# Kernel tuning notes

Measured on AMD Instinct MI355X. Metric: run time of the kernel, lower is better.

Reference implementation:

```python
import jax, jax.numpy as jnp
import numpy as np

CPG = 2          # channels_per_group
WH, WW = 227, 227  # window_size
EPS = 1e-05


def setup_inputs() -> dict:
    key = jax.random.key(0)
    x = jax.random.normal(key, (8, 32, 512, 512), dtype=jnp.float32)
    weight = jnp.ones((1, 32, 1, 1), dtype=jnp.float32)
    bias = jnp.zeros((1, 32, 1, 1), dtype=jnp.float32)
    return {"x": x, "weight": weight, "bias": bias}


def _box_sum(ii, wh, ww):
    # ii: integral image (N,C,H,W); returns window sums of size (wh,ww)
    # over rows h+1..h+wh, cols w+1..w+ww -> (N,C,H-wh,W-ww)
    return (ii[:, :, wh:, ww:] - ii[:, :, :-wh, ww:]
            - ii[:, :, wh:, :-ww] + ii[:, :, :-wh, :-ww])


def reference(x, weight, bias):
    N, C, H, W = x.shape
    G = C // CPG
    # window_size (227,227) < (H,W)=(512,512): integral-image branch
    ii = jnp.cumsum(jnp.cumsum(x, axis=2), axis=3)
    ii_sq = jnp.cumsum(jnp.cumsum(x * x, axis=2), axis=3)
    h, w = H - WH, W - WW
    # per-channel box sums, then sum over channels_per_group -> (N,G,h,w)
    sums = _box_sum(ii, WH, WW).reshape(N, G, CPG, h, w).sum(axis=2)
    squares = _box_sum(ii_sq, WH, WW).reshape(N, G, CPG, h, w).sum(axis=2)
    n = WH * WW * CPG
    means = sums / n
    var = (squares - sums * sums / n) / n
    # replicate-pad stats back to (H,W): (left,right,top,bottom) like F.pad
    pt, pb = (H - h) // 2, H - h - (H - h) // 2
    pl, pr = (W - w) // 2, W - w - (W - w) // 2
    pad = ((0, 0), (0, 0), (pt, pb), (pl, pr))
    p_means = jnp.pad(means, pad, mode='edge')
    p_vars = jnp.pad(var, pad, mode='edge') + EPS
    # torch computes sums/squares under no_grad -> stats are constants
    p_means = jax.lax.stop_gradient(p_means)
    p_vars = jax.lax.stop_gradient(p_vars)
    xg = x.reshape(N, G, CPG, H, W)
    out = (xg - p_means[:, :, None]) / jnp.sqrt(p_vars)[:, :, None]
    out = out.reshape(N, C, H, W)
    return out * weight + bias
```

## Files before the change

kernel.cpp:

```cpp
#include <hip/hip_runtime.h>

namespace {
constexpr int Hn = 512, Wn = 512;
constexpr int WHn = 227, WWn = 227;
constexpr int OHn = 285, OWn = 285;
constexpr int PTn = 113, PLn = 113;
constexpr float EPSn = 1e-5f;
constexpr int NSEG = 17, NSLOT = 9;
__device__ __constant__ int kSegA[NSEG] =
    {1,37,73,109,145,181,217,228,253,264,285,300,336,372,408,444,480};
__device__ __constant__ int kSegB[NSEG] =
    {36,72,108,144,180,216,227,252,263,284,299,335,371,407,443,479,511};
__device__ __constant__ int kWinLo[NSLOT] = {0,1,2,3,4,5,6,8,10};
__device__ __constant__ int kWinHi[NSLOT] = {6,8,10,11,12,13,14,15,16};
__device__ __constant__ int kBr0[8] = {0,29,57,85,398,427,456,484};
__device__ __constant__ int kBrN[8] = {29,28,28,28,29,29,28,28};
}

__global__ __launch_bounds__(512, 4) void lcn_snap(const float* __restrict__ x,
                                                   float2* __restrict__ snap) {
  const int B = blockIdx.x;
  const int g = B >> 2;
  const int st = B & 3;
  const int w = threadIdx.x;
  const int q2 = w & 31;
  const int p = w >> 5;

  const float4* __restrict__ b0 =
      reinterpret_cast<const float4*>(x + (size_t)(g * 2) * Hn * Wn) + st * 32 + q2;
  const float4* __restrict__ b1 = b0 + (size_t)Hn * (Wn / 4);

  __shared__ float4 tbuf[16][64];
  __shared__ float2 segLds[NSEG][128];

  for (int s = 0; s < NSEG; ++s) {
    float4 aS = {0.f,0.f,0.f,0.f}, aQ = {0.f,0.f,0.f,0.f};
    for (int r = kSegA[s] + p; r <= kSegB[s]; r += 16) {
      float4 a = b0[(size_t)r * (Wn / 4)];
      float4 b = b1[(size_t)r * (Wn / 4)];
      aS.x += a.x + b.x; aQ.x += a.x * a.x + b.x * b.x;
      aS.y += a.y + b.y; aQ.y += a.y * a.y + b.y * b.y;
      aS.z += a.z + b.z; aQ.z += a.z * a.z + b.z * b.z;
      aS.w += a.w + b.w; aQ.w += a.w * a.w + b.w * b.w;
    }
    __syncthreads();
    tbuf[p][2 * q2]     = make_float4(aS.x, aQ.x, aS.y, aQ.y);
    tbuf[p][2 * q2 + 1] = make_float4(aS.z, aQ.z, aS.w, aQ.w);
    __syncthreads();
    if (w < 128) {
      const float2* cf = reinterpret_cast<const float2*>(&tbuf[0][0]);
      float2 acc = {0.f, 0.f};
      #pragma unroll
      for (int pp = 0; pp < 16; ++pp) {
        float2 t = cf[pp * 128 + w];
        acc.x += t.x; acc.y += t.y;
      }
      segLds[s][w] = acc;
    }
  }
  __syncthreads();
  if (w < 128) {
    for (int k = 0; k < NSLOT; ++k) {
      float2 acc = {0.f, 0.f};
      for (int i = kWinLo[k]; i <= kWinHi[k]; ++i) {
        acc.x += segLds[i][w].x; acc.y += segLds[i][w].y;
      }
      snap[((size_t)g * NSLOT + k) * 512 + st * 128 + w] = acc;
    }
  }
}

__global__ __launch_bounds__(512, 4) void lcn_fused(const float* __restrict__ x,
                                                    const float* __restrict__ weight,
                                                    const float* __restrict__ bias,
                                                    const float2* __restrict__ snap,
                                                    float* __restrict__ out) {
  const int B = blockIdx.x;
  const int X = B & 7;
  const int s = B >> 3;
  const int chunk = s & 7;
  const int g = X * 16 + (s >> 3);
  const int w = threadIdx.x;
  const int lane = w & 63;
  const int wid = w >> 6;

  const float* __restrict__ x0 = x + (size_t)(g * 2) * Hn * Wn;
  const float* __restrict__ x1 = x0 + (size_t)Hn * Wn;
  float* __restrict__ o0 = out + (size_t)(g * 2) * Hn * Wn;
  float* __restrict__ o1 = o0 + (size_t)Hn * Wn;
  const int cch = (g & 15) * 2;
  const float wt0 = weight[cch], wt1 = weight[cch + 1];
  const float bs0 = bias[cch], bs1 = bias[cch + 1];

  const int h0 = chunk * 36;
  const int h1 = min(OHn, h0 + 36);

  __shared__ __align__(16) float2 Ps[2][4][Wn + 1];
  __shared__ float2 wsum[8][4];

  const float2 sv = snap[((size_t)g * NSLOT + chunk) * 512 + w];
  float accS = sv.x, accQ = sv.y;
  const int bslot = (chunk < 4) ? 0 : 8;
  const float2 bv = snap[((size_t)g * NSLOT + bslot) * 512 + w];

  const float inv_n = 1.0f / (float)(WHn * WWn * 2);
  const int wp = min(max(w - PLn, 0), OWn - 1);

  float pa0[4], pa1[4], ps0[4], ps1[4];
  auto prefetch = [&](int hb) {
    #pragma unroll
    for (int j = 0; j < 4; ++j) {
      int ra = min(hb + WHn + 1 + j, Hn - 1);
      int rs = hb + 1 + j;
      pa0[j] = x0[(size_t)ra * Wn + w];
      pa1[j] = x1[(size_t)ra * Wn + w];
      ps0[j] = x0[(size_t)rs * Wn + w];
      ps1[j] = x1[(size_t)rs * Wn + w];
    }
  };
  prefetch(h0);

  int buf = 0;
  for (int h = h0; h < h1; h += 4) {
    float2 v[4];
    v[0] = make_float2(accS, accQ);
    float s2 = accS, q2 = accQ;
    #pragma unroll
    for (int j = 0; j < 3; ++j) {
      s2 += (pa0[j] + pa1[j]) - (ps0[j] + ps1[j]);
      q2 += (pa0[j] * pa0[j] + pa1[j] * pa1[j])
          - (ps0[j] * ps0[j] + ps1[j] * ps1[j]);
      v[j + 1] = make_float2(s2, q2);
    }
    s2 += (pa0[3] + pa1[3]) - (ps0[3] + ps1[3]);
    q2 += (pa0[3] * pa0[3] + pa1[3] * pa1[3])
        - (ps0[3] * ps0[3] + ps1[3] * ps1[3]);
    accS = s2; accQ = q2;

    if (h + 4 < h1) prefetch(h + 4);
    float xa[4], xb[4];
    #pragma unroll
    for (int rr = 0; rr < 4; ++rr) {
      const size_t hh = (size_t)(h + PTn + rr) * Wn + w;
      xa[rr] = x0[hh];
      xb[rr] = x1[hh];
    }

    #pragma unroll
    for (int d = 1; d < 64; d <<= 1) {
      #pragma unroll
      for (int rr = 0; rr < 4; ++rr) {
        float sx = __shfl_up(v[rr].x, d, 64);
        float sy = __shfl_up(v[rr].y, d, 64);
        if (lane >= d) { v[rr].x += sx; v[rr].y += sy; }
      }
    }
    if (lane == 63) {
      #pragma unroll
      for (int rr = 0; rr < 4; ++rr) wsum[wid][rr] = v[rr];
    }
    __syncthreads();
    float2 off[4] = {{0.f,0.f},{0.f,0.f},{0.f,0.f},{0.f,0.f}};
    #pragma unroll
    for (int i = 0; i < 7; ++i) {
      if (i < wid) {
        #pragma unroll
        for (int rr = 0; rr < 4; ++rr) {
          off[rr].x += wsum[i][rr].x; off[rr].y += wsum[i][rr].y;
        }
      }
    }
    #pragma unroll
    for (int rr = 0; rr < 4; ++rr)
      Ps[buf][rr][w + 1] = make_float2(v[rr].x + off[rr].x, v[rr].y + off[rr].y);
    __syncthreads();

    #pragma unroll
    for (int rr = 0; rr < 4; ++rr) {
      if (h + rr < h1) {
        float2 hi = Ps[buf][rr][wp + WWn + 1];
        float2 lo = Ps[buf][rr][wp + 1];
        float S = hi.x - lo.x;
        float Q = hi.y - lo.y;
        float mean = S * inv_n;
        float var = (Q - S * S * inv_n) * inv_n;
        float istd = rsqrtf(var + EPSn);
        const size_t oo = (size_t)(h + PTn + rr) * Wn + w;
        o0[oo] = (xa[rr] - mean) * istd * wt0 + bs0;
        o1[oo] = (xb[rr] - mean) * istd * wt1 + bs1;
      }
    }
    buf ^= 1;
  }

  __syncthreads();
  {
    float2 v = bv;
    #pragma unroll
    for (int d = 1; d < 64; d <<= 1) {
      float sx = __shfl_up(v.x, d, 64);
      float sy = __shfl_up(v.y, d, 64);
      if (lane >= d) { v.x += sx; v.y += sy; }
    }
    if (lane == 63) wsum[wid][0] = v;
    __syncthreads();
    float2 off = {0.f, 0.f};
    #pragma unroll
    for (int i = 0; i < 7; ++i) {
      if (i < wid) { off.x += wsum[i][0].x; off.y += wsum[i][0].y; }
    }
    Ps[0][0][w + 1] = make_float2(v.x + off.x, v.y + off.y);
    __syncthreads();
    float2 hi = Ps[0][0][wp + WWn + 1];
    float2 lo = Ps[0][0][wp + 1];
    float S = hi.x - lo.x;
    float Q = hi.y - lo.y;
    float mean = S * inv_n;
    float var = (Q - S * S * inv_n) * inv_n;
    float istd = rsqrtf(var + EPSn);
    Ps[0][1][w] = make_float2(mean, istd);
    __syncthreads();
  }
  {
    const float2* bst = &Ps[0][1][0];
    const int row0 = kBr0[chunk];
    const int total = kBrN[chunk] * 256;
    const float4* __restrict__ xf0 = reinterpret_cast<const float4*>(x0);
    const float4* __restrict__ xf1 = reinterpret_cast<const float4*>(x1);
    float4* __restrict__ of0 = reinterpret_cast<float4*>(o0);
    float4* __restrict__ of1 = reinterpret_cast<float4*>(o1);
    for (int i = w; i < total; i += 512) {
      const int qq = i & 127;
      const int ch = (i >> 7) & 1;
      const int row = row0 + (i >> 8);
      const size_t idx = (size_t)row * (Wn / 4) + qq;
      const float4 xv = ch ? xf1[idx] : xf0[idx];
      const float wt = ch ? wt1 : wt0;
      const float bsv = ch ? bs1 : bs0;
      const float2 m0 = bst[4 * qq + 0];
      const float2 m1 = bst[4 * qq + 1];
      const float2 m2 = bst[4 * qq + 2];
      const float2 m3 = bst[4 * qq + 3];
      float4 ov;
      ov.x = (xv.x - m0.x) * m0.y * wt + bsv;
      ov.y = (xv.y - m1.x) * m1.y * wt + bsv;
      ov.z = (xv.z - m2.x) * m2.y * wt + bsv;
      ov.w = (xv.w - m3.x) * m3.y * wt + bsv;
      if (ch) of1[idx] = ov; else of0[idx] = ov;
    }
  }
}

extern "C" void kernel_launch(void* const* d_in, const int* in_sizes, int n_in,
                              void* d_out, int out_size, void* d_ws, size_t ws_size,
                              hipStream_t stream) {
  const float* x = (const float*)d_in[0];
  const float* weight = (const float*)d_in[1];
  const float* bias = (const float*)d_in[2];
  float* out = (float*)d_out;
  float2* snap = (float2*)d_ws;

  hipLaunchKernelGGL(lcn_snap, dim3(512), dim3(512), 0, stream, x, snap);
  hipLaunchKernelGGL(lcn_fused, dim3(1024), dim3(512), 0, stream,
                     x, weight, bias, snap, out);
}
```

Before: 180.8 us.

## Write padded border rows from prefetched sliding-window registers instead of re-reading

The replicate-padded top and bottom border rows are now computed inside the main sliding-window loop, reusing the rows already prefetched for the running-sum update instead of running a separate epilogue pass that re-reads x for those rows. The border mean/istd is computed once up front, and row 0 is handled separately by chunk 0. The snap kernel's column reduction loop is also unrolled by two to keep more loads in flight. This removes redundant global reads, but the border stores are now scattered per row inside the loop and are only done by the chunks that happen to cover those rows.

```diff
diff --git a/kernel.cpp b/kernel.cpp
--- a/kernel.cpp
+++ b/kernel.cpp
@@ -13,8 +13,6 @@
     {36,72,108,144,180,216,227,252,263,284,299,335,371,407,443,479,511};
 __device__ __constant__ int kWinLo[NSLOT] = {0,1,2,3,4,5,6,8,10};
 __device__ __constant__ int kWinHi[NSLOT] = {6,8,10,11,12,13,14,15,16};
-__device__ __constant__ int kBr0[8] = {0,29,57,85,398,427,456,484};
-__device__ __constant__ int kBrN[8] = {29,28,28,28,29,29,28,28};
 }
 
 __global__ __launch_bounds__(512, 4) void lcn_snap(const float* __restrict__ x,
@@ -35,13 +33,26 @@
 
   for (int s = 0; s < NSEG; ++s) {
     float4 aS = {0.f,0.f,0.f,0.f}, aQ = {0.f,0.f,0.f,0.f};
-    for (int r = kSegA[s] + p; r <= kSegB[s]; r += 16) {
+    const int rA = kSegA[s] + p, rB = kSegB[s];
+    for (int r = rA; r <= rB; r += 32) {
       float4 a = b0[(size_t)r * (Wn / 4)];
       float4 b = b1[(size_t)r * (Wn / 4)];
+      const bool sec = (r + 16 <= rB);
+      float4 c, d;
+      if (sec) {
+        c = b0[(size_t)(r + 16) * (Wn / 4)];
+        d = b1[(size_t)(r + 16) * (Wn / 4)];
+      }
       aS.x += a.x + b.x; aQ.x += a.x * a.x + b.x * b.x;
       aS.y += a.y + b.y; aQ.y += a.y * a.y + b.y * b.y;
       aS.z += a.z + b.z; aQ.z += a.z * a.z + b.z * b.z;
       aS.w += a.w + b.w; aQ.w += a.w * a.w + b.w * b.w;
+      if (sec) {
+        aS.x += c.x + d.x; aQ.x += c.x * c.x + d.x * d.x;
+        aS.y += c.y + d.y; aQ.y += c.y * c.y + d.y * d.y;
+        aS.z += c.z + d.z; aQ.z += c.z * c.z + d.z * d.z;
+        aS.w += c.w + d.w; aQ.w += c.w * c.w + d.w * d.w;
+      }
     }
     __syncthreads();
     tbuf[p][2 * q2]     = make_float4(aS.x, aQ.x, aS.y, aQ.y);
@@ -106,6 +117,37 @@
   const float inv_n = 1.0f / (float)(WHn * WWn * 2);
   const int wp = min(max(w - PLn, 0), OWn - 1);
 
+  float mean_b, istd_b;
+  {
+    float2 v = bv;
+    #pragma unroll
+    for (int d = 1; d < 64; d <<= 1) {
+      float sx = __shfl_up(v.x, d, 64);
+      float sy = __shfl_up(v.y, d, 64);
+      if (lane >= d) { v.x += sx; v.y += sy; }
+    }
+    if (lane == 63) wsum[wid][0] = v;
+    __syncthreads();
+    float2 off = {0.f, 0.f};
+    #pragma unroll
+    for (int i = 0; i < 7; ++i) {
+      if (i < wid) { off.x += wsum[i][0].x; off.y += wsum[i][0].y; }
+    }
+    Ps[0][0][w + 1] = make_float2(v.x + off.x, v.y + off.y);
+    __syncthreads();
+    float2 hi = Ps[0][0][wp + WWn + 1];
+    float2 lo = Ps[0][0][wp + 1];
+    float S = hi.x - lo.x;
+    float Q = hi.y - lo.y;
+    mean_b = S * inv_n;
+    istd_b = rsqrtf((Q - S * S * inv_n) * inv_n + EPSn);
+  }
+  if (chunk == 0) {
+    float a = x0[w], b = x1[w];
+    o0[w] = (a - mean_b) * istd_b * wt0 + bs0;
+    o1[w] = (b - mean_b) * istd_b * wt1 + bs1;
+  }
+
   float pa0[4], pa1[4], ps0[4], ps1[4];
   auto prefetch = [&](int hb) {
     #pragma unroll
@@ -136,6 +178,13 @@
     q2 += (pa0[3] * pa0[3] + pa1[3] * pa1[3])
         - (ps0[3] * ps0[3] + ps1[3] * ps1[3]);
     accS = s2; accQ = q2;
+
+    float bb0[4], bb1[4];
+    #pragma unroll
+    for (int j = 0; j < 4; ++j) {
+      bb0[j] = (chunk < 4) ? ps0[j] : pa0[j];
+      bb1[j] = (chunk < 4) ? ps1[j] : pa1[j];
+    }
 
     if (h + 4 < h1) prefetch(h + 4);
     float xa[4], xb[4];
@@ -190,64 +239,18 @@
         o1[oo] = (xb[rr] - mean) * istd * wt1 + bs1;
       }
     }
+
+    #pragma unroll
+    for (int j = 0; j < 4; ++j) {
+      const int r = (chunk < 4) ? (h + 1 + j) : (h + WHn + 1 + j);
+      const bool duty = (chunk < 4) ? (r <= 112) : (r >= 398 && r <= 511);
+      if (duty) {
+        const size_t oo = (size_t)r * Wn + w;
+        o0[oo] = (bb0[j] - mean_b) * istd_b * wt0 + bs0;
+        o1[oo] = (bb1[j] - mean_b) * istd_b * wt1 + bs1;
+      }
+    }
     buf ^= 1;
-  }
-
-  __syncthreads();
-  {
-    float2 v = bv;
-    #pragma unroll
-    for (int d = 1; d < 64; d <<= 1) {
-      float sx = __shfl_up(v.x, d, 64);
-      float sy = __shfl_up(v.y, d, 64);
-      if (lane >= d) { v.x += sx; v.y += sy; }
-    }
-    if (lane == 63) wsum[wid][0] = v;
-    __syncthreads();
-    float2 off = {0.f, 0.f};
-    #pragma unroll
-    for (int i = 0; i < 7; ++i) {
-      if (i < wid) { off.x += wsum[i][0].x; off.y += wsum[i][0].y; }
-    }
-    Ps[0][0][w + 1] = make_float2(v.x + off.x, v.y + off.y);
-    __syncthreads();
-    float2 hi = Ps[0][0][wp + WWn + 1];
-    float2 lo = Ps[0][0][wp + 1];
-    float S = hi.x - lo.x;
-    float Q = hi.y - lo.y;
-    float mean = S * inv_n;
-    float var = (Q - S * S * inv_n) * inv_n;
-    float istd = rsqrtf(var + EPSn);
-    Ps[0][1][w] = make_float2(mean, istd);
-    __syncthreads();
-  }
-  {
-    const float2* bst = &Ps[0][1][0];
-    const int row0 = kBr0[chunk];
-    const int total = kBrN[chunk] * 256;
-    const float4* __restrict__ xf0 = reinterpret_cast<const float4*>(x0);
-    const float4* __restrict__ xf1 = reinterpret_cast<const float4*>(x1);
-    float4* __restrict__ of0 = reinterpret_cast<float4*>(o0);
-    float4* __restrict__ of1 = reinterpret_cast<float4*>(o1);
-    for (int i = w; i < total; i += 512) {
-      const int qq = i & 127;
-      const int ch = (i >> 7) & 1;
-      const int row = row0 + (i >> 8);
-      const size_t idx = (size_t)row * (Wn / 4) + qq;
-      const float4 xv = ch ? xf1[idx] : xf0[idx];
-      const float wt = ch ? wt1 : wt0;
-      const float bsv = ch ? bs1 : bs0;
-      const float2 m0 = bst[4 * qq + 0];
-      const float2 m1 = bst[4 * qq + 1];
-      const float2 m2 = bst[4 * qq + 2];
-      const float2 m3 = bst[4 * qq + 3];
-      float4 ov;
-      ov.x = (xv.x - m0.x) * m0.y * wt + bsv;
-      ov.y = (xv.y - m1.x) * m1.y * wt + bsv;
-      ov.z = (xv.z - m2.x) * m2.y * wt + bsv;
-      ov.w = (xv.w - m3.x) * m3.y * wt + bsv;
-      if (ch) of1[idx] = ov; else of0[idx] = ov;
-    }
   }
 }
 
```

Measured after the change: 168.1 us, median of 2. -7.0%, faster.
